# Performance work log

Hardware: AMD Instinct MI355X
Metric: run time of the kernel (lower is better)

The kernel has to match this reference:

```python
import jax, jax.numpy as jnp
import numpy as np

PATCH = 7          # patch_size (stride fixed to 1, loop=False)
ALPHA = 0.01       # coherent_alpha


def extract_patches(x, p):
    # x: [1, C, T] -> [n, C*p], n = T - p + 1  (unfold over time, stride 1)
    b, c, t = x.shape
    n = t - p + 1
    idx = jnp.arange(n)[:, None] + jnp.arange(p)[None, :]   # [n, p]
    patches = x[0][:, idx]                                   # [C, n, p]
    return patches.transpose(1, 0, 2).reshape(n, c * p)      # [n, C*p]


def setup_inputs() -> dict:
    key = jax.random.key(0)
    kx, ky = jax.random.split(key)
    X = jax.random.normal(kx, (1, 72, 8192), dtype=jnp.float32)
    Y = jax.random.normal(ky, (1, 72, 8192), dtype=jnp.float32)
    return {"X": X, "Y": Y}


def reference(X, Y):
    p = PATCH
    b, c, t = X.shape
    d = c * p
    xp = extract_patches(X, p)                               # [n1, d]
    yp = extract_patches(Y, p)                               # [n2, d]
    # efficient_cdist: squared L2 distances, normalized by patch dim d
    dist = ((xp * xp).sum(1)[:, None] + (yp * yp).sum(1)[None, :]
            - 2.0 * (xp @ yp.T)) / d                         # [n1, n2]
    # coherent_alpha: bidirectional-similarity normalization by per-y-patch min
    norm_dist = dist / (ALPHA + dist.min(axis=0, keepdims=True))
    nnf = jnp.argmin(norm_dist, axis=1)                      # [n1] int
    dists = jnp.take_along_axis(dist, nnf[:, None], axis=1)[:, 0]
    # combine_patches: gather matched y patches, overlap-add (fold), normalize by counts
    matched = yp[nnf].reshape(-1, c, p)                      # [n1, C, p]
    n1 = matched.shape[0]
    idx = jnp.arange(n1)[:, None] + jnp.arange(p)[None, :]   # [n1, p] -> time index
    acc = jnp.zeros((c, t), X.dtype).at[:, idx].add(matched.transpose(1, 0, 2))
    cnt = jnp.zeros((t,), X.dtype).at[idx].add(jnp.ones((n1, p), X.dtype))
    blended = (acc / cnt)[None]                              # [1, C, T]
    return blended, dists.mean()
```

## Files before the change

kernel.cpp:

```cpp
#include <hip/hip_runtime.h>
#include <stdint.h>

#define TT 8192
#define CC 72
#define PP 7
#define NN (TT - PP + 1)
#define DD (CC * PP)

#define TI 122
#define SG 128
#define SPAD 132
#define NTILE ((NN + TI - 1) / TI)

#define STAGE_BYTES (CC * SG * 4)
#define SMEM_UNION  (2 * STAGE_BYTES)

#define TAIL_BYTES 196608

constexpr float INV_D = 1.0f / (float)DD;
constexpr float ALPHA_C = 0.01f;

__global__ void prep_kernel(const float* __restrict__ X, const float* __restrict__ Y,
                            float* __restrict__ sx, float* __restrict__ sy,
                            unsigned* __restrict__ colmin,
                            unsigned long long* __restrict__ packed,
                            float* __restrict__ dsum) {
    int i = blockIdx.x * 256 + threadIdx.x;
    if (i == 0) *dsum = 0.0f;
    if (i < TT) { colmin[i] = 0x7f800000u; packed[i] = ~0ULL; }
    if (i < NN) {
        float ax = 0.0f, ay = 0.0f;
        for (int c = 0; c < CC; ++c) {
            const float* xr = X + c * TT + i;
            const float* yr = Y + c * TT + i;
#pragma unroll
            for (int k = 0; k < PP; ++k) {
                float v = xr[k]; ax += v * v;
                float w = yr[k]; ay += w * w;
            }
        }
        sx[i] = ax; sy[i] = ay;
    }
}

__device__ __forceinline__ void tile_dots(const float* __restrict__ X,
                                          const float* __restrict__ Y,
                                          int i0, int j0, char* smem,
                                          float dot[8][8]) {
    float (*Xs)[SG]   = (float (*)[SG])smem;
    float (*Ys)[SG]   = (float (*)[SG])(smem + STAGE_BYTES);
    float (*Sl)[SPAD] = (float (*)[SPAD])smem;
    const int tid = threadIdx.x;

    for (int idx = tid; idx < CC * SG / 2; idx += 256) {
        int c  = idx >> 6;
        int t2 = (idx & 63) * 2;
        int gx = i0 + t2, gy = j0 + t2;
        float2 xv, yv;
        if (gx + 1 < TT) xv = *(const float2*)(X + c * TT + gx);
        else { xv.x = X[c * TT + min(gx, TT - 1)]; xv.y = X[c * TT + min(gx + 1, TT - 1)]; }
        if (gy + 1 < TT) yv = *(const float2*)(Y + c * TT + gy);
        else { yv.x = Y[c * TT + min(gy, TT - 1)]; yv.y = Y[c * TT + min(gy + 1, TT - 1)]; }
        *(float2*)&Xs[c][t2] = xv;
        *(float2*)&Ys[c][t2] = yv;
    }
    __syncthreads();

    const int su = tid >> 4, sv = tid & 15;
    float s[8][8];
#pragma unroll
    for (int a = 0; a < 8; ++a)
#pragma unroll
        for (int b = 0; b < 8; ++b) s[a][b] = 0.0f;

#pragma unroll 4
    for (int c = 0; c < CC; ++c) {
        float xv[8], yv[8];
        *(float4*)&xv[0] = *(const float4*)&Xs[c][su * 8];
        *(float4*)&xv[4] = *(const float4*)&Xs[c][su * 8 + 4];
        *(float4*)&yv[0] = *(const float4*)&Ys[c][sv * 4];
        *(float4*)&yv[4] = *(const float4*)&Ys[c][64 + sv * 4];
#pragma unroll
        for (int a = 0; a < 8; ++a)
#pragma unroll
            for (int b = 0; b < 8; ++b)
                s[a][b] += xv[a] * yv[b];
    }
    __syncthreads();

#pragma unroll
    for (int a = 0; a < 8; ++a) {
        int row = su * 8 + a;
        int swz = ((row >> 3) & 3) << 2;
        *(float4*)&Sl[row][(sv * 4) ^ swz]      = make_float4(s[a][0], s[a][1], s[a][2], s[a][3]);
        *(float4*)&Sl[row][(64 + sv * 4) ^ swz] = make_float4(s[a][4], s[a][5], s[a][6], s[a][7]);
    }
    __syncthreads();

    const int ri = (tid >> 4) * 8, rj = (tid & 15) * 8;
#pragma unroll
    for (int a = 0; a < 8; ++a)
#pragma unroll
        for (int b = 0; b < 8; ++b) dot[a][b] = 0.0f;

#pragma unroll
    for (int r = 0; r < 14; ++r) {
        int row = ri + r;
        int swz = ((row >> 3) & 3) << 2;
        float f[14];
        *(float4*)&f[0]  = *(const float4*)&Sl[row][(rj)      ^ swz];
        *(float4*)&f[4]  = *(const float4*)&Sl[row][(rj + 4)  ^ swz];
        *(float4*)&f[8]  = *(const float4*)&Sl[row][(rj + 8)  ^ swz];
        *(float2*)&f[12] = *(const float2*)&Sl[row][(rj + 12) ^ swz];
#pragma unroll
        for (int a = 0; a < 8; ++a) {
            const int k = r - a;
            if (k >= 0 && k < PP) {
#pragma unroll
                for (int b = 0; b < 8; ++b)
                    dot[a][b] += f[b + k];
            }
        }
    }
}

__global__ __launch_bounds__(256) void pass1_k(
        const float* __restrict__ X, const float* __restrict__ Y,
        const float* __restrict__ sx, const float* __restrict__ sy,
        unsigned* __restrict__ colmin,
        float* __restrict__ distbuf, int storeTiles) {
    __shared__ __align__(16) char smem[SMEM_UNION + 1024];
    unsigned* cmin_s = (unsigned*)(smem + SMEM_UNION);

    const int i0 = blockIdx.y * TI;
    const int j0 = blockIdx.x * TI;
    const int tid = threadIdx.x;
    const bool store = ((int)blockIdx.y < storeTiles);
    if (tid < 128) cmin_s[tid] = 0x7f800000u;

    float dot[8][8];
    tile_dots(X, Y, i0, j0, smem, dot);

    const int ri = (tid >> 4) * 8, rj = (tid & 15) * 8;
    const int gj0 = j0 + rj;

    bool bv[8]; float syv[8];
#pragma unroll
    for (int b = 0; b < 8; ++b) {
        int lj = rj + b, gj = gj0 + b;
        bv[b] = (lj < TI && gj < NN);
        syv[b] = bv[b] ? sy[gj] : 0.0f;
    }
    const bool fullCols = (rj + 7 < TI) && (gj0 + 7 < NN);
    const bool al16 = ((gj0 & 3) == 0);

    float cm[8];
#pragma unroll
    for (int b = 0; b < 8; ++b) cm[b] = __uint_as_float(0x7f800000u);

#pragma unroll
    for (int a = 0; a < 8; ++a) {
        int li = ri + a, gi = i0 + li;
        if (li >= TI || gi >= NN) continue;
        float sxi = sx[gi];
        float d8[8];
#pragma unroll
        for (int b = 0; b < 8; ++b) {
            d8[b] = (sxi + syv[b] - 2.0f * dot[a][b]) * INV_D;
            if (bv[b]) cm[b] = fminf(cm[b], d8[b]);
        }
        if (store) {
            float* drow = distbuf + (size_t)gi * TT + gj0;
            if (fullCols) {
                if (al16) {
                    *(float4*)&drow[0] = make_float4(d8[0], d8[1], d8[2], d8[3]);
                    *(float4*)&drow[4] = make_float4(d8[4], d8[5], d8[6], d8[7]);
                } else {
                    *(float2*)&drow[0] = make_float2(d8[0], d8[1]);
                    *(float4*)&drow[2] = make_float4(d8[2], d8[3], d8[4], d8[5]);
                    *(float2*)&drow[6] = make_float2(d8[6], d8[7]);
                }
            } else {
#pragma unroll
                for (int b = 0; b < 8; ++b)
                    if (bv[b]) drow[b] = d8[b];
            }
        }
    }
#pragma unroll
    for (int b = 0; b < 8; ++b)
        if (bv[b]) atomicMin(&cmin_s[rj + b], __float_as_uint(cm[b]));
    __syncthreads();
    if (tid < TI) {
        int gj = j0 + tid;
        if (gj < NN) atomicMin(&colmin[gj], cmin_s[tid]);
    }
}

template<bool FULL>
__global__ __launch_bounds__(256) void pass2_stream_k(
        const float* __restrict__ distbuf, const unsigned* __restrict__ colmin,
        unsigned long long* __restrict__ packed,
        int* __restrict__ nnf, float* __restrict__ dists) {
    const int i = blockIdx.x;
    const float* row = distbuf + (size_t)i * TT;
    const float* cmf = (const float*)colmin;

    unsigned long long best = ~0ULL;
    for (int jb = threadIdx.x * 8; jb < NN; jb += 2048) {
        float4 d4a = *(const float4*)(row + jb);
        float4 d4b = *(const float4*)(row + jb + 4);
        float4 c4a = *(const float4*)(cmf + jb);
        float4 c4b = *(const float4*)(cmf + jb + 4);
#pragma unroll
        for (int e = 0; e < 8; ++e) {
            int j = jb + e;
            if (j < NN) {
                float d   = (e < 4) ? (&d4a.x)[e] : (&d4b.x)[e - 4];
                float cmv = (e < 4) ? (&c4a.x)[e] : (&c4b.x)[e - 4];
                float nd  = d / (ALPHA_C + cmv);
                unsigned long long pk =
                    ((unsigned long long)__float_as_uint(nd) << 32) | (unsigned)j;
                best = (pk < best) ? pk : best;
            }
        }
    }
#pragma unroll
    for (int off = 32; off > 0; off >>= 1) {
        unsigned long long o = __shfl_down(best, off, 64);
        best = (o < best) ? o : best;
    }
    __shared__ unsigned long long wb[4];
    int lane = threadIdx.x & 63, wid = threadIdx.x >> 6;
    if (lane == 0) wb[wid] = best;
    __syncthreads();
    if (threadIdx.x == 0) {
        unsigned long long b0 = wb[0];
        b0 = (wb[1] < b0) ? wb[1] : b0;
        b0 = (wb[2] < b0) ? wb[2] : b0;
        b0 = (wb[3] < b0) ? wb[3] : b0;
        if (FULL) {
            int j = (int)(b0 & 0xffffffffu);
            nnf[i]   = j;
            dists[i] = row[j];
        } else {
            packed[i] = b0;
        }
    }
}

__global__ __launch_bounds__(256) void meansum_kernel(
        const float* __restrict__ dists, float* __restrict__ dsum) {
    float s = 0.0f;
    for (int i = threadIdx.x; i < NN; i += 256) s += dists[i];
    __shared__ float red[256];
    red[threadIdx.x] = s;
    __syncthreads();
    for (int st = 128; st > 0; st >>= 1) {
        if (threadIdx.x < st) red[threadIdx.x] += red[threadIdx.x + st];
        __syncthreads();
    }
    if (threadIdx.x == 0) *dsum = red[0];
}

__global__ __launch_bounds__(256) void pass2_k(
        const float* __restrict__ X, const float* __restrict__ Y,
        const float* __restrict__ sx, const float* __restrict__ sy,
        const unsigned* __restrict__ colmin,
        unsigned long long* __restrict__ packed, int itile_ofs) {
    __shared__ __align__(16) char smem[SMEM_UNION + 1024];
    unsigned long long* pmin_s = (unsigned long long*)(smem + SMEM_UNION);

    const int i0 = (itile_ofs + blockIdx.y) * TI;
    const int j0 = blockIdx.x * TI;
    const int tid = threadIdx.x;
    if (tid < TI) pmin_s[tid] = ~0ULL;

    float dot[8][8];
    tile_dots(X, Y, i0, j0, smem, dot);

    const int ri = (tid >> 4) * 8, rj = (tid & 15) * 8;
    const int gj0 = j0 + rj;

    bool bv[8]; float syv[8], acm[8];
#pragma unroll
    for (int b = 0; b < 8; ++b) {
        int lj = rj + b, gj = gj0 + b;
        bv[b] = (lj < TI && gj < NN);
        syv[b] = bv[b] ? sy[gj] : 0.0f;
        acm[b] = bv[b] ? (ALPHA_C + __uint_as_float(colmin[gj])) : 1.0f;
    }

#pragma unroll
    for (int a = 0; a < 8; ++a) {
        int li = ri + a, gi = i0 + li;
        if (li >= TI || gi >= NN) continue;
        float sxi = sx[gi];
        unsigned long long best = ~0ULL;
#pragma unroll
        for (int b = 0; b < 8; ++b) {
            if (bv[b]) {
                float d  = (sxi + syv[b] - 2.0f * dot[a][b]) * INV_D;
                float nd = d / acm[b];
                unsigned long long pk =
                    ((unsigned long long)__float_as_uint(nd) << 32) | (unsigned)(gj0 + b);
                best = (pk < best) ? pk : best;
            }
        }
        atomicMin(&pmin_s[li], best);
    }
    __syncthreads();
    if (tid < TI) {
        int gi = i0 + tid;
        if (gi < NN) atomicMin(&packed[gi], pmin_s[tid]);
    }
}

__global__ void finalize_kernel(const float* __restrict__ X, const float* __restrict__ Y,
                                const float* __restrict__ sx, const float* __restrict__ sy,
                                const unsigned long long* __restrict__ packed,
                                int* __restrict__ nnf, float* __restrict__ dsum) {
    int i = blockIdx.x * 256 + threadIdx.x;
    float dval = 0.0f;
    if (i < NN) {
        int j = (int)(packed[i] & 0xffffffffu);
        nnf[i] = j;
        float dot = 0.0f;
        for (int c = 0; c < CC; ++c) {
            const float* xr = X + c * TT + i;
            const float* yr = Y + c * TT + j;
#pragma unroll
            for (int k = 0; k < PP; ++k) dot += xr[k] * yr[k];
        }
        dval = (sx[i] + sy[j] - 2.0f * dot) * INV_D;
    }
    __shared__ float red[256];
    red[threadIdx.x] = dval;
    __syncthreads();
    for (int s = 128; s > 0; s >>= 1) {
        if (threadIdx.x < s) red[threadIdx.x] += red[threadIdx.x + s];
        __syncthreads();
    }
    if (threadIdx.x == 0) atomicAdd(dsum, red[0]);
}

__global__ void fold_kernel(const float* __restrict__ Y, const int* __restrict__ nnf,
                            const float* __restrict__ dsum, float* __restrict__ out) {
    int idx = blockIdx.x * 256 + threadIdx.x;
    if (idx < CC * TT) {
        int c = idx >> 13;
        int t = idx & (TT - 1);
        float acc = 0.0f;
        int cnt = 0;
#pragma unroll
        for (int k = 0; k < PP; ++k) {
            int i = t - k;
            if (i >= 0 && i < NN) {
                acc += Y[c * TT + nnf[i] + k];
                cnt++;
            }
        }
        out[idx] = acc / (float)cnt;
    }
    if (idx == 0) out[CC * TT] = *dsum / (float)NN;
}

extern "C" void kernel_launch(void* const* d_in, const int* in_sizes, int n_in,
                              void* d_out, int out_size, void* d_ws, size_t ws_size,
                              hipStream_t stream) {
    const float* X = (const float*)d_in[0];
    const float* Y = (const float*)d_in[1];
    float* out = (float*)d_out;

    char* w = (char*)d_ws;
    size_t base = 0;
    if (ws_size > TAIL_BYTES) base = ((ws_size - TAIL_BYTES) / 32768) * 32768;
    unsigned long long* packed = (unsigned long long*)(w + base);
    float*              dists  = (float*)(w + base);
    unsigned*           colmin = (unsigned*)(w + base + 65536);
    float*              sx     = (float*)(w + base + 98304);
    float*              sy     = (float*)(w + base + 131072);
    int*                nnf    = (int*)(w + base + 163840);
    float*              dsum   = (float*)(w + base + 196600);
    float*              distbuf = (float*)w;

    const long storeRows = (long)(base / ((size_t)TT * 4));
    int storeTiles = 0;
    for (int nT = 1; nT <= NTILE; ++nT) {
        long need = (long)nT * TI; if (need > NN) need = NN;
        if (need <= storeRows) storeTiles = nT; else break;
    }
    const int SR = (storeTiles * TI < NN) ? storeTiles * TI : NN;
    const bool full = (storeTiles >= NTILE);

    prep_kernel<<<(TT + 255) / 256, 256, 0, stream>>>(X, Y, sx, sy, colmin, packed, dsum);

    dim3 grid(NTILE, NTILE);
    pass1_k<<<grid, 256, 0, stream>>>(X, Y, sx, sy, colmin, distbuf, storeTiles);

    if (full) {
        pass2_stream_k<true><<<NN, 256, 0, stream>>>(distbuf, colmin, packed, nnf, dists);
        meansum_kernel<<<1, 256, 0, stream>>>(dists, dsum);
    } else {
        if (SR > 0)
            pass2_stream_k<false><<<SR, 256, 0, stream>>>(distbuf, colmin, packed, nnf, dists);
        if (storeTiles < NTILE) {
            dim3 grid2(NTILE, NTILE - storeTiles);
            pass2_k<<<grid2, 256, 0, stream>>>(X, Y, sx, sy, colmin, packed, storeTiles);
        }
        finalize_kernel<<<(NN + 255) / 256, 256, 0, stream>>>(X, Y, sx, sy, packed, nnf, dsum);
    }
    fold_kernel<<<(CC * TT + 255) / 256, 256, 0, stream>>>(Y, nnf, dsum, out);
}
```

Measured before the change: 327.0 us.

## Use 512-thread pass1 blocks, split prep over X/Y, fuse mean via fixed-point atomics

The distance-tile kernel now runs 512 threads per block, with each thread computing a 4x8 output block instead of 8x8. This halves per-thread register pressure and adds more waves per tile. The prep kernel splits the X and Y squared-norm computations across two grid rows to double its parallelism. The separate single-block mean reduction kernel is removed: each row adds its matched distance into a 64-bit fixed-point accumulator with atomics, which keeps the sum deterministic but quantises the values to 2^-26.

```diff
diff --git a/kernel.cpp b/kernel.cpp
--- a/kernel.cpp
+++ b/kernel.cpp
@@ -19,34 +19,123 @@
 
 constexpr float INV_D = 1.0f / (float)DD;
 constexpr float ALPHA_C = 0.01f;
+constexpr float QSCALE = 67108864.0f;
 
 __global__ void prep_kernel(const float* __restrict__ X, const float* __restrict__ Y,
                             float* __restrict__ sx, float* __restrict__ sy,
                             unsigned* __restrict__ colmin,
                             unsigned long long* __restrict__ packed,
-                            float* __restrict__ dsum) {
+                            unsigned long long* __restrict__ qsum) {
     int i = blockIdx.x * 256 + threadIdx.x;
-    if (i == 0) *dsum = 0.0f;
-    if (i < TT) { colmin[i] = 0x7f800000u; packed[i] = ~0ULL; }
-    if (i < NN) {
-        float ax = 0.0f, ay = 0.0f;
-        for (int c = 0; c < CC; ++c) {
-            const float* xr = X + c * TT + i;
-            const float* yr = Y + c * TT + i;
-#pragma unroll
-            for (int k = 0; k < PP; ++k) {
-                float v = xr[k]; ax += v * v;
-                float w = yr[k]; ay += w * w;
-            }
-        }
-        sx[i] = ax; sy[i] = ay;
-    }
-}
-
-__device__ __forceinline__ void tile_dots(const float* __restrict__ X,
-                                          const float* __restrict__ Y,
-                                          int i0, int j0, char* smem,
-                                          float dot[8][8]) {
+    if (blockIdx.y == 0) {
+        if (i == 0) *qsum = 0ULL;
+        if (i < TT) { colmin[i] = 0x7f800000u; packed[i] = ~0ULL; }
+        if (i < NN) {
+            float ax = 0.0f;
+            for (int c = 0; c < CC; ++c) {
+                const float* xr = X + c * TT + i;
+#pragma unroll
+                for (int k = 0; k < PP; ++k) { float v = xr[k]; ax += v * v; }
+            }
+            sx[i] = ax;
+        }
+    } else {
+        if (i < NN) {
+            float ay = 0.0f;
+            for (int c = 0; c < CC; ++c) {
+                const float* yr = Y + c * TT + i;
+#pragma unroll
+                for (int k = 0; k < PP; ++k) { float w = yr[k]; ay += w * w; }
+            }
+            sy[i] = ay;
+        }
+    }
+}
+
+__device__ __forceinline__ void tile_dots512(const float* __restrict__ X,
+                                             const float* __restrict__ Y,
+                                             int i0, int j0, char* smem,
+                                             float dot[4][8]) {
+    float (*Xs)[SG]   = (float (*)[SG])smem;
+    float (*Ys)[SG]   = (float (*)[SG])(smem + STAGE_BYTES);
+    float (*Sl)[SPAD] = (float (*)[SPAD])smem;
+    const int tid = threadIdx.x;
+
+    for (int idx = tid; idx < CC * SG / 2; idx += 512) {
+        int c  = idx >> 6;
+        int t2 = (idx & 63) * 2;
+        int gx = i0 + t2, gy = j0 + t2;
+        float2 xv, yv;
+        if (gx + 1 < TT) xv = *(const float2*)(X + c * TT + gx);
+        else { xv.x = X[c * TT + min(gx, TT - 1)]; xv.y = X[c * TT + min(gx + 1, TT - 1)]; }
+        if (gy + 1 < TT) yv = *(const float2*)(Y + c * TT + gy);
+        else { yv.x = Y[c * TT + min(gy, TT - 1)]; yv.y = Y[c * TT + min(gy + 1, TT - 1)]; }
+        *(float2*)&Xs[c][t2] = xv;
+        *(float2*)&Ys[c][t2] = yv;
+    }
+    __syncthreads();
+
+    const int su = tid >> 4, sv = tid & 15;
+    float s[4][8];
+#pragma unroll
+    for (int a = 0; a < 4; ++a)
+#pragma unroll
+        for (int b = 0; b < 8; ++b) s[a][b] = 0.0f;
+
+#pragma unroll 4
+    for (int c = 0; c < CC; ++c) {
+        float xv[4], yv[8];
+        *(float4*)&xv[0] = *(const float4*)&Xs[c][su * 4];
+        *(float4*)&yv[0] = *(const float4*)&Ys[c][sv * 4];
+        *(float4*)&yv[4] = *(const float4*)&Ys[c][64 + sv * 4];
+#pragma unroll
+        for (int a = 0; a < 4; ++a)
+#pragma unroll
+            for (int b = 0; b < 8; ++b)
+                s[a][b] += xv[a] * yv[b];
+    }
+    __syncthreads();
+
+#pragma unroll
+    for (int a = 0; a < 4; ++a) {
+        int row = su * 4 + a;
+        int swz = ((row >> 3) & 3) << 2;
+        *(float4*)&Sl[row][(sv * 4) ^ swz]      = make_float4(s[a][0], s[a][1], s[a][2], s[a][3]);
+        *(float4*)&Sl[row][(64 + sv * 4) ^ swz] = make_float4(s[a][4], s[a][5], s[a][6], s[a][7]);
+    }
+    __syncthreads();
+
+    const int ri = (tid >> 4) * 4, rj = (tid & 15) * 8;
+#pragma unroll
+    for (int a = 0; a < 4; ++a)
+#pragma unroll
+        for (int b = 0; b < 8; ++b) dot[a][b] = 0.0f;
+
+#pragma unroll
+    for (int r = 0; r < 10; ++r) {
+        int row = ri + r;
+        int swz = ((row >> 3) & 3) << 2;
+        float f[14];
+        *(float4*)&f[0]  = *(const float4*)&Sl[row][(rj)      ^ swz];
+        *(float4*)&f[4]  = *(const float4*)&Sl[row][(rj + 4)  ^ swz];
+        *(float4*)&f[8]  = *(const float4*)&Sl[row][(rj + 8)  ^ swz];
+        *(float2*)&f[12] = *(const float2*)&Sl[row][(rj + 12) ^ swz];
+#pragma unroll
+        for (int a = 0; a < 4; ++a) {
+            const int k = r - a;
+            if (k >= 0 && k < PP) {
+#pragma unroll
+                for (int b = 0; b < 8; ++b)
+                    dot[a][b] += f[b + k];
+            }
+        }
+    }
+}
+
+__device__ __forceinline__ void tile_dots256(const float* __restrict__ X,
+                                             const float* __restrict__ Y,
+                                             int i0, int j0, char* smem,
+                                             float dot[8][8]) {
     float (*Xs)[SG]   = (float (*)[SG])smem;
     float (*Ys)[SG]   = (float (*)[SG])(smem + STAGE_BYTES);
     float (*Sl)[SPAD] = (float (*)[SPAD])smem;
@@ -124,7 +213,7 @@
     }
 }
 
-__global__ __launch_bounds__(256) void pass1_k(
+__global__ __launch_bounds__(512) void pass1_k(
         const float* __restrict__ X, const float* __restrict__ Y,
         const float* __restrict__ sx, const float* __restrict__ sy,
         unsigned* __restrict__ colmin,
@@ -138,10 +227,10 @@
     const bool store = ((int)blockIdx.y < storeTiles);
     if (tid < 128) cmin_s[tid] = 0x7f800000u;
 
-    float dot[8][8];
-    tile_dots(X, Y, i0, j0, smem, dot);
-
-    const int ri = (tid >> 4) * 8, rj = (tid & 15) * 8;
+    float dot[4][8];
+    tile_dots512(X, Y, i0, j0, smem, dot);
+
+    const int ri = (tid >> 4) * 4, rj = (tid & 15) * 8;
     const int gj0 = j0 + rj;
 
     bool bv[8]; float syv[8];
@@ -159,7 +248,7 @@
     for (int b = 0; b < 8; ++b) cm[b] = __uint_as_float(0x7f800000u);
 
 #pragma unroll
-    for (int a = 0; a < 8; ++a) {
+    for (int a = 0; a < 4; ++a) {
         int li = ri + a, gi = i0 + li;
         if (li >= TI || gi >= NN) continue;
         float sxi = sx[gi];
@@ -201,7 +290,7 @@
 __global__ __launch_bounds__(256) void pass2_stream_k(
         const float* __restrict__ distbuf, const unsigned* __restrict__ colmin,
         unsigned long long* __restrict__ packed,
-        int* __restrict__ nnf, float* __restrict__ dists) {
+        int* __restrict__ nnf, unsigned long long* __restrict__ qsum) {
     const int i = blockIdx.x;
     const float* row = distbuf + (size_t)i * TT;
     const float* cmf = (const float*)colmin;
@@ -241,26 +330,13 @@
         b0 = (wb[3] < b0) ? wb[3] : b0;
         if (FULL) {
             int j = (int)(b0 & 0xffffffffu);
-            nnf[i]   = j;
-            dists[i] = row[j];
+            nnf[i] = j;
+            float dval = row[j];
+            atomicAdd(qsum, (unsigned long long)(long long)(dval * QSCALE));
         } else {
             packed[i] = b0;
         }
     }
-}
-
-__global__ __launch_bounds__(256) void meansum_kernel(
-        const float* __restrict__ dists, float* __restrict__ dsum) {
-    float s = 0.0f;
-    for (int i = threadIdx.x; i < NN; i += 256) s += dists[i];
-    __shared__ float red[256];
-    red[threadIdx.x] = s;
-    __syncthreads();
-    for (int st = 128; st > 0; st >>= 1) {
-        if (threadIdx.x < st) red[threadIdx.x] += red[threadIdx.x + st];
-        __syncthreads();
-    }
-    if (threadIdx.x == 0) *dsum = red[0];
 }
 
 __global__ __launch_bounds__(256) void pass2_k(
@@ -277,7 +353,7 @@
     if (tid < TI) pmin_s[tid] = ~0ULL;
 
     float dot[8][8];
-    tile_dots(X, Y, i0, j0, smem, dot);
+    tile_dots256(X, Y, i0, j0, smem, dot);
 
     const int ri = (tid >> 4) * 8, rj = (tid & 15) * 8;
     const int gj0 = j0 + rj;
@@ -319,9 +395,9 @@
 __global__ void finalize_kernel(const float* __restrict__ X, const float* __restrict__ Y,
                                 const float* __restrict__ sx, const float* __restrict__ sy,
                                 const unsigned long long* __restrict__ packed,
-                                int* __restrict__ nnf, float* __restrict__ dsum) {
+                                int* __restrict__ nnf, unsigned long long* __restrict__ qsum) {
     int i = blockIdx.x * 256 + threadIdx.x;
-    float dval = 0.0f;
+    long long q = 0;
     if (i < NN) {
         int j = (int)(packed[i] & 0xffffffffu);
         nnf[i] = j;
@@ -332,20 +408,22 @@
 #pragma unroll
             for (int k = 0; k < PP; ++k) dot += xr[k] * yr[k];
         }
-        dval = (sx[i] + sy[j] - 2.0f * dot) * INV_D;
-    }
-    __shared__ float red[256];
-    red[threadIdx.x] = dval;
+        float dval = (sx[i] + sy[j] - 2.0f * dot) * INV_D;
+        q = (long long)(dval * QSCALE);
+    }
+    __shared__ long long red[256];
+    red[threadIdx.x] = q;
     __syncthreads();
     for (int s = 128; s > 0; s >>= 1) {
         if (threadIdx.x < s) red[threadIdx.x] += red[threadIdx.x + s];
         __syncthreads();
     }
-    if (threadIdx.x == 0) atomicAdd(dsum, red[0]);
+    if (threadIdx.x == 0) atomicAdd(qsum, (unsigned long long)red[0]);
 }
 
 __global__ void fold_kernel(const float* __restrict__ Y, const int* __restrict__ nnf,
-                            const float* __restrict__ dsum, float* __restrict__ out) {
+                            const unsigned long long* __restrict__ qsum,
+                            float* __restrict__ out) {
     int idx = blockIdx.x * 256 + threadIdx.x;
     if (idx < CC * TT) {
         int c = idx >> 13;
@@ -362,7 +440,10 @@
         }
         out[idx] = acc / (float)cnt;
     }
-    if (idx == 0) out[CC * TT] = *dsum / (float)NN;
+    if (idx == 0) {
+        double m = (double)*qsum * (1.0 / (double)QSCALE) / (double)NN;
+        out[CC * TT] = (float)m;
+    }
 }
 
 extern "C" void kernel_launch(void* const* d_in, const int* in_sizes, int n_in,
@@ -376,12 +457,11 @@
     size_t base = 0;
     if (ws_size > TAIL_BYTES) base = ((ws_size - TAIL_BYTES) / 32768) * 32768;
     unsigned long long* packed = (unsigned long long*)(w + base);
-    float*              dists  = (float*)(w + base);
     unsigned*           colmin = (unsigned*)(w + base + 65536);
     float*              sx     = (float*)(w + base + 98304);
     float*              sy     = (float*)(w + base + 131072);
     int*                nnf    = (int*)(w + base + 163840);
-    float*              dsum   = (float*)(w + base + 196600);
+    unsigned long long* qsum   = (unsigned long long*)(w + base + 196600);
     float*              distbuf = (float*)w;
 
     const long storeRows = (long)(base / ((size_t)TT * 4));
@@ -393,22 +473,21 @@
     const int SR = (storeTiles * TI < NN) ? storeTiles * TI : NN;
     const bool full = (storeTiles >= NTILE);
 
-    prep_kernel<<<(TT + 255) / 256, 256, 0, stream>>>(X, Y, sx, sy, colmin, packed, dsum);
+    prep_kernel<<<dim3((TT + 255) / 256, 2), 256, 0, stream>>>(X, Y, sx, sy, colmin, packed, qsum);
 
     dim3 grid(NTILE, NTILE);
-    pass1_k<<<grid, 256, 0, stream>>>(X, Y, sx, sy, colmin, distbuf, storeTiles);
+    pass1_k<<<grid, 512, 0, stream>>>(X, Y, sx, sy, colmin, distbuf, storeTiles);
 
     if (full) {
-        pass2_stream_k<true><<<NN, 256, 0, stream>>>(distbuf, colmin, packed, nnf, dists);
-        meansum_kernel<<<1, 256, 0, stream>>>(dists, dsum);
+        pass2_stream_k<true><<<NN, 256, 0, stream>>>(distbuf, colmin, packed, nnf, qsum);
     } else {
         if (SR > 0)
-            pass2_stream_k<false><<<SR, 256, 0, stream>>>(distbuf, colmin, packed, nnf, dists);
+            pass2_stream_k<false><<<SR, 256, 0, stream>>>(distbuf, colmin, packed, nnf, qsum);
         if (storeTiles < NTILE) {
             dim3 grid2(NTILE, NTILE - storeTiles);
             pass2_k<<<grid2, 256, 0, stream>>>(X, Y, sx, sy, colmin, packed, storeTiles);
         }
-        finalize_kernel<<<(NN + 255) / 256, 256, 0, stream>>>(X, Y, sx, sy, packed, nnf, dsum);
-    }
-    fold_kernel<<<(CC * TT + 255) / 256, 256, 0, stream>>>(Y, nnf, dsum, out);
-}
+        finalize_kernel<<<(NN + 255) / 256, 256, 0, stream>>>(X, Y, sx, sy, packed, nnf, qsum);
+    }
+    fold_kernel<<<(CC * TT + 255) / 256, 256, 0, stream>>>(Y, nnf, qsum, out);
+}
```

After: 417.3 us. 27.6% more time.
